# Performance work log

Measured on AMD Instinct MI355X. Metric: run time of the kernel, lower is better.

The kernel has to match this reference:

```python
import jax, jax.numpy as jnp
import numpy as np

B, S, D, H, DK = 32, 1024, 256, 8, 32
MASK_VALUE = -1e-30  # note: NOT -inf; masked scores become ~0 pre-softmax, faithful to source


def setup_inputs() -> dict:
    key = jax.random.key(0)
    ks = jax.random.split(key, 7)
    query = jax.random.normal(ks[0], (B, S, D), dtype=jnp.float32)
    key_t = jax.random.normal(ks[1], (B, S, D), dtype=jnp.float32)
    value = jax.random.normal(ks[2], (B, S, D), dtype=jnp.float32)
    # binary observation mask over key positions
    mask = (jax.random.uniform(ks[3], (B, S)) > 0.5).astype(jnp.float32)
    glorot = jax.nn.initializers.glorot_uniform(in_axis=1, out_axis=2)
    Wq = glorot(ks[4], (H, D, DK), jnp.float32)
    Wk = glorot(ks[5], (H, D, DK), jnp.float32)
    Wv = glorot(ks[6], (H, D, DK), jnp.float32)
    return {"query": query, "key": key_t, "value": value, "mask": mask,
            "Wq": Wq, "Wk": Wk, "Wv": Wv}


def reference(query, key, value, mask, Wq, Wk, Wv):
    # per-head projections, vectorized over heads: [B,S,D] x [H,D,DK] -> [B,H,S,DK]
    q = jnp.einsum('bsd,hdk->bhsk', query, Wq)
    k = jnp.einsum('bsd,hdk->bhsk', key, Wk)
    v = jnp.einsum('bsd,hdk->bhsk', value, Wv)
    # raw scores (no 1/sqrt(dk) scaling in source): [B,H,Sq,Sk]
    A = jnp.einsum('bhqk,bhsk->bhqs', q, k)
    m = mask[:, None, None, :]  # [B,1,1,Sk]
    A = m * A + (1.0 - m) * MASK_VALUE  # multiplicative mask, NOT additive
    A = jax.nn.softmax(A, axis=-1)
    out = jnp.einsum('bhqs,bhsk->bhqk', A, v)  # [B,H,Sq,DK]
    # concat heads along last dim, matching torch.cat order
    return out.transpose(0, 2, 1, 3).reshape(B, S, H * DK)
```

## Files before the change

### kernel.cpp

```cpp
#include <hip/hip_runtime.h>
#include <math.h>

#define B_  32
#define S_  1024
#define D_  256
#define H_  8
#define DK_ 32
#define MASKV (-1e-30f)
#define LOG2E 1.44269504f

typedef __attribute__((ext_vector_type(4))) short bf4_t;
typedef __attribute__((ext_vector_type(8))) short bf8_t;
typedef __attribute__((ext_vector_type(4))) float f4_t;

__device__ __forceinline__ unsigned fbits(float x) {
    union { float f; unsigned u; } v; v.f = x; return v.u;
}
__device__ __forceinline__ float bitsf(unsigned u) {
    union { unsigned u; float f; } v; v.u = u; return v.f;
}

#if __has_builtin(__builtin_amdgcn_exp2f)
#define EXP2F(x) __builtin_amdgcn_exp2f(x)
#else
#define EXP2F(x) __expf((x) * 0.69314718f)
#endif

__device__ __forceinline__ void gld16(const void* g, void* l) {
    __builtin_amdgcn_global_load_lds(
        (const __attribute__((address_space(1))) void*)g,
        (__attribute__((address_space(3))) void*)l, 16, 0, 0);
}

#define PSEL 0x07060302u

__global__ __launch_bounds__(256) void prep_w(
    const float* __restrict__ Wq, const float* __restrict__ Wk,
    const float* __restrict__ Wv, short* __restrict__ WtH, short* __restrict__ WtL)
{
    const int a = blockIdx.x >> 3;
    const int h = blockIdx.x & 7;
    const float* W = (a == 0 ? Wq : (a == 1 ? Wk : Wv)) + (size_t)h * 256 * 32;
    const int t = threadIdx.x;
    const int k    = t & 31;
    const int dgrp = t >> 5;
    short* th = WtH + ((size_t)a * 256 + h * 32 + k) * 256;
    short* tl = WtL + ((size_t)a * 256 + h * 32 + k) * 256;
#pragma unroll
    for (int jj = blockIdx.y * 2; jj < blockIdx.y * 2 + 2; ++jj) {
        const int d0 = jj * 32 + dgrp * 4;
        float x[4];
#pragma unroll
        for (int r = 0; r < 4; ++r) x[r] = W[(size_t)(d0 + r) * 32 + k];
        unsigned hu[4], lu[4];
#pragma unroll
        for (int r = 0; r < 4; ++r) {
            unsigned hb = (fbits(x[r]) + 0x8000u) & 0xFFFF0000u;
            hu[r] = hb;
            lu[r] = fbits(x[r] - bitsf(hb)) + 0x8000u;
        }
        uint2 hp = make_uint2(__builtin_amdgcn_perm(hu[1], hu[0], PSEL),
                              __builtin_amdgcn_perm(hu[3], hu[2], PSEL));
        uint2 lp = make_uint2(__builtin_amdgcn_perm(lu[1], lu[0], PSEL),
                              __builtin_amdgcn_perm(lu[3], lu[2], PSEL));
        *(uint2*)&th[d0] = hp;
        *(uint2*)&tl[d0] = lp;
    }
}

__global__ __launch_bounds__(256) void proj_kernel(
    const float* __restrict__ Xq, const float* __restrict__ Xk,
    const float* __restrict__ Xv,
    const short* __restrict__ WtH, const short* __restrict__ WtL,
    short* __restrict__ qpH, short* __restrict__ qpL,
    short* __restrict__ kpH, short* __restrict__ kpL,
    short* __restrict__ vpT)
{
    __shared__ __align__(16) short XsH[64 * 32];
    __shared__ __align__(16) short XsL[64 * 32];
    __shared__ __align__(16) short WsH[256 * 32];
    __shared__ __align__(16) short WsL[256 * 32];

    const int a  = blockIdx.y;
    const float* X = (a == 0 ? Xq : (a == 1 ? Xk : Xv));
    const short* WH = WtH + (size_t)a * 256 * 256;
    const short* WL = WtL + (size_t)a * 256 * 256;
    const int m0 = blockIdx.x * 64;

    const int tid  = threadIdx.x;
    const int lane = tid & 63;
    const int wv   = tid >> 6;
    const int l15  = lane & 15;
    const int quad = lane >> 4;

    f4_t acc[4][4];
#pragma unroll
    for (int i = 0; i < 4; ++i)
#pragma unroll
        for (int j = 0; j < 4; ++j) acc[i][j] = (f4_t){0.f, 0.f, 0.f, 0.f};

    for (int kc = 0; kc < 8; ++kc) {
        __syncthreads();
        {
            const float* xp = X + (size_t)(m0 + (tid >> 2)) * 256 + kc * 32 + (tid & 3) * 8;
            float4 x0 = *(const float4*)xp;
            float4 x1 = *(const float4*)(xp + 4);
            float xv[8] = {x0.x, x0.y, x0.z, x0.w, x1.x, x1.y, x1.z, x1.w};
            bf8_t hi, lo;
#pragma unroll
            for (int j = 0; j < 8; ++j) {
                unsigned hu = (fbits(xv[j]) + 0x8000u) & 0xFFFF0000u;
                hi[j] = (short)(hu >> 16);
                lo[j] = (short)((fbits(xv[j] - bitsf(hu)) + 0x8000u) >> 16);
            }
            *(bf8_t*)&XsH[(tid >> 2) * 32 + (tid & 3) * 8] = hi;
            *(bf8_t*)&XsL[(tid >> 2) * 32 + (tid & 3) * 8] = lo;
        }
#pragma unroll
        for (int i = 0; i < 4; ++i) {
            size_t go = (size_t)((i * 4 + wv) * 16 + (lane >> 2)) * 256 + kc * 32 + (lane & 3) * 8;
            gld16(WH + go, (char*)WsH + (i * 4 + wv) * 1024);
            gld16(WL + go, (char*)WsL + (i * 4 + wv) * 1024);
        }
        __syncthreads();

        bf8_t wH[4], wL[4];
#pragma unroll
        for (int ns = 0; ns < 4; ++ns) {
            int n = wv * 64 + ns * 16 + l15;
            wH[ns] = *(const bf8_t*)&WsH[n * 32 + quad * 8];
            wL[ns] = *(const bf8_t*)&WsL[n * 32 + quad * 8];
        }
#pragma unroll
        for (int t = 0; t < 4; ++t) {
            bf8_t xH = *(const bf8_t*)&XsH[(t * 16 + l15) * 32 + quad * 8];
            bf8_t xL = *(const bf8_t*)&XsL[(t * 16 + l15) * 32 + quad * 8];
#pragma unroll
            for (int ns = 0; ns < 4; ++ns) {
                f4_t c = acc[t][ns];
                if (a < 2) {
                    c = __builtin_amdgcn_mfma_f32_16x16x32_bf16(wH[ns], xH, c, 0, 0, 0);
                    c = __builtin_amdgcn_mfma_f32_16x16x32_bf16(wL[ns], xH, c, 0, 0, 0);
                    c = __builtin_amdgcn_mfma_f32_16x16x32_bf16(wH[ns], xL, c, 0, 0, 0);
                } else {
                    c = __builtin_amdgcn_mfma_f32_16x16x32_bf16(xH, wH[ns], c, 0, 0, 0);
                    c = __builtin_amdgcn_mfma_f32_16x16x32_bf16(xH, wL[ns], c, 0, 0, 0);
                    c = __builtin_amdgcn_mfma_f32_16x16x32_bf16(xL, wH[ns], c, 0, 0, 0);
                }
                acc[t][ns] = c;
            }
        }
    }

    const int b  = m0 >> 10;
    const int sB = m0 & 1023;
    if (a < 2) {
        short* dH = (a == 0) ? qpH : kpH;
        short* dL = (a == 0) ? qpL : kpL;
        const float scale = (a == 0) ? LOG2E : 1.0f;
#pragma unroll
        for (int t = 0; t < 4; ++t) {
            int s = sB + t * 16 + l15;
#pragma unroll
            for (int ns = 0; ns < 4; ++ns) {
                int nw = wv * 64 + ns * 16 + quad * 4;
                int h = nw >> 5, k0 = nw & 31;
                unsigned hu[4], lu[4];
#pragma unroll
                for (int r = 0; r < 4; ++r) {
                    float x = acc[t][ns][r] * scale;
                    unsigned h32 = fbits(x) + 0x8000u;
                    hu[r] = h32;
                    float hf = bitsf(h32 & 0xFFFF0000u);
                    lu[r] = fbits(x - hf) + 0x8000u;
                }
                uint2 hp = make_uint2(__builtin_amdgcn_perm(hu[1], hu[0], PSEL),
                                      __builtin_amdgcn_perm(hu[3], hu[2], PSEL));
                uint2 lp = make_uint2(__builtin_amdgcn_perm(lu[1], lu[0], PSEL),
                                      __builtin_amdgcn_perm(lu[3], lu[2], PSEL));
                size_t off = ((size_t)(b * 8 + h) * 1024 + s) * 32 + k0;
                *(uint2*)&dH[off] = hp;
                *(uint2*)&dL[off] = lp;
            }
        }
    } else {
#pragma unroll
        for (int t = 0; t < 4; ++t) {
            int sr = sB + t * 16 + quad * 4;
#pragma unroll
            for (int ns = 0; ns < 4; ++ns) {
                int n = wv * 64 + ns * 16 + l15;
                int h = n >> 5, k = n & 31;
                unsigned eu[4];
#pragma unroll
                for (int r = 0; r < 4; ++r) eu[r] = fbits(acc[t][ns][r]) + 0x8000u;
                uint2 pk = make_uint2(__builtin_amdgcn_perm(eu[1], eu[0], PSEL),
                                      __builtin_amdgcn_perm(eu[3], eu[2], PSEL));
                *(uint2*)&vpT[((size_t)(b * 8 + h) * 32 + k) * 1024 + sr] = pk;
            }
        }
    }
}

__global__ __launch_bounds__(256) void attn_kernel(
    const short* __restrict__ qpH, const short* __restrict__ qpL,
    const short* __restrict__ kpH, const short* __restrict__ kpL,
    const short* __restrict__ vpT, const float* __restrict__ mask,
    float* __restrict__ out)
{
    __shared__ __align__(16) short KsH[64 * 32];
    __shared__ __align__(16) short KsL[64 * 32];
    __shared__ __align__(16) short VsT[32 * 72];
    __shared__ __align__(16) float mskM[64];
    __shared__ __align__(16) float mskC[64];

    const int tid  = threadIdx.x;
    const int lane = tid & 63;
    const int wv   = tid >> 6;
    const int l15  = lane & 15;
    const int quad = lane >> 4;

    const int qt = blockIdx.x;
    const int h  = blockIdx.y;
    const int b  = blockIdx.z;
    const int bh = b * 8 + h;
    const int woff = qt * 128 + wv * 32;

    bf8_t qh[2], ql[2];
#pragma unroll
    for (int qs = 0; qs < 2; ++qs) {
        size_t row = (size_t)bh * 1024 + woff + qs * 16 + l15;
        qh[qs] = *(const bf8_t*)&qpH[row * 32 + quad * 8];
        ql[qs] = *(const bf8_t*)&qpL[row * 32 + quad * 8];
    }

    f4_t accO[2][2];
    f4_t accS[2];
#pragma unroll
    for (int i = 0; i < 2; ++i) {
        accS[i] = (f4_t){0.f, 0.f, 0.f, 0.f};
#pragma unroll
        for (int j = 0; j < 2; ++j) accO[i][j] = (f4_t){0.f, 0.f, 0.f, 0.f};
    }
    const bf4_t ones4 = {(short)0x3F80, (short)0x3F80, (short)0x3F80, (short)0x3F80};

    const float* mb = mask + (size_t)b * 1024;

    for (int kt = 0; kt < 16; ++kt) {
        __syncthreads();
        {
            size_t toff = ((size_t)bh * 1024 + kt * 64) * 32;
            gld16(kpH + toff + wv * 512 + lane * 8, (char*)KsH + wv * 1024);
            gld16(kpL + toff + wv * 512 + lane * 8, (char*)KsL + wv * 1024);
        }
        {
            int dv = tid >> 3, seg = tid & 7;
            const uint4 vvv = *(const uint4*)&vpT[((size_t)bh * 32 + dv) * 1024 + kt * 64 + seg * 8];
            *(uint4*)&VsT[dv * 72 + seg * 8] = vvv;
        }
        if (tid < 64) {
            float m = mb[kt * 64 + tid];
            mskM[tid] = m;
            mskC[tid] = (1.f - m) * (MASKV * LOG2E);
        }
        __syncthreads();

        f4_t sc[2][4];
#pragma unroll
        for (int ks = 0; ks < 4; ++ks) {
            bf8_t kh = *(const bf8_t*)&KsH[(ks * 16 + l15) * 32 + quad * 8];
            bf8_t kl = *(const bf8_t*)&KsL[(ks * 16 + l15) * 32 + quad * 8];
#pragma unroll
            for (int qs = 0; qs < 2; ++qs) {
                f4_t c = __builtin_amdgcn_mfma_f32_16x16x32_bf16(kh, qh[qs],
                             (f4_t){0.f, 0.f, 0.f, 0.f}, 0, 0, 0);
                c = __builtin_amdgcn_mfma_f32_16x16x32_bf16(kl, qh[qs], c, 0, 0, 0);
                c = __builtin_amdgcn_mfma_f32_16x16x32_bf16(kh, ql[qs], c, 0, 0, 0);
                sc[qs][ks] = c;
            }
        }

        bf4_t pf[2][4];
#pragma unroll
        for (int ks = 0; ks < 4; ++ks) {
            float4 m4 = *(const float4*)&mskM[ks * 16 + quad * 4];
            float4 c4 = *(const float4*)&mskC[ks * 16 + quad * 4];
            float mr[4] = {m4.x, m4.y, m4.z, m4.w};
            float cr[4] = {c4.x, c4.y, c4.z, c4.w};
#pragma unroll
            for (int qs = 0; qs < 2; ++qs) {
                unsigned eu[4];
#pragma unroll
                for (int r = 0; r < 4; ++r) {
                    float sm = fmaf(sc[qs][ks][r], mr[r], cr[r]);
                    eu[r] = fbits(EXP2F(sm)) + 0x8000u;
                }
                union { uint2 u; bf4_t v; } cv;
                cv.u = make_uint2(__builtin_amdgcn_perm(eu[1], eu[0], PSEL),
                                  __builtin_amdgcn_perm(eu[3], eu[2], PSEL));
                pf[qs][ks] = cv.v;
            }
        }

#pragma unroll
        for (int ks = 0; ks < 4; ++ks) {
            bf4_t vf0 = *(const bf4_t*)&VsT[l15 * 72 + ks * 16 + quad * 4];
            bf4_t vf1 = *(const bf4_t*)&VsT[(16 + l15) * 72 + ks * 16 + quad * 4];
#pragma unroll
            for (int qs = 0; qs < 2; ++qs) {
                accO[qs][0] = __builtin_amdgcn_mfma_f32_16x16x16bf16_1k(vf0, pf[qs][ks], accO[qs][0], 0, 0, 0);
                accO[qs][1] = __builtin_amdgcn_mfma_f32_16x16x16bf16_1k(vf1, pf[qs][ks], accO[qs][1], 0, 0, 0);
                accS[qs]    = __builtin_amdgcn_mfma_f32_16x16x16bf16_1k(ones4, pf[qs][ks], accS[qs], 0, 0, 0);
            }
        }
    }

#pragma unroll
    for (int qs = 0; qs < 2; ++qs) {
        float inv = 1.0f / accS[qs][0];
        int s = woff + qs * 16 + l15;
        float* op = out + ((size_t)b * 1024 + s) * 256 + h * 32;
#pragma unroll
        for (int dvs = 0; dvs < 2; ++dvs) {
            float4 o4 = make_float4(accO[qs][dvs][0] * inv, accO[qs][dvs][1] * inv,
                                    accO[qs][dvs][2] * inv, accO[qs][dvs][3] * inv);
            *(float4*)&op[dvs * 16 + quad * 4] = o4;
        }
    }
}

extern "C" void kernel_launch(void* const* d_in, const int* in_sizes, int n_in,
                              void* d_out, int out_size, void* d_ws, size_t ws_size,
                              hipStream_t stream)
{
    const float* query = (const float*)d_in[0];
    const float* key   = (const float*)d_in[1];
    const float* value = (const float*)d_in[2];
    const float* mask  = (const float*)d_in[3];
    const float* Wq    = (const float*)d_in[4];
    const float* Wk    = (const float*)d_in[5];
    const float* Wv    = (const float*)d_in[6];
    float* out = (float*)d_out;

    const size_t per = (size_t)B_ * H_ * S_ * DK_;
    short* qpH = (short*)d_ws;
    short* qpL = qpH + per;
    short* kpH = qpL + per;
    short* kpL = kpH + per;
    short* vpT = kpL + per;
    short* WtH = vpT + per;
    short* WtL = WtH + 3 * 256 * 256;

    prep_w<<<dim3(24, 4), 256, 0, stream>>>(Wq, Wk, Wv, WtH, WtL);
    proj_kernel<<<dim3(512, 3), 256, 0, stream>>>(query, key, value, WtH, WtL,
                                                  qpH, qpL, kpH, kpL, vpT);
    attn_kernel<<<dim3(8, H_, B_), 256, 0, stream>>>(qpH, qpL, kpH, kpL, vpT, mask, out);
}
```

Measured before the change: 284.2 us.

## Fold key mask into K projection and double-buffer K/V tiles in attention

The key mask is now multiplied into the K projection output inside proj_kernel. The attention kernel therefore drops its per-tile mask loads and the mask FMA. Masked scores become exactly 0 instead of roughly -1e-30, which gives the same exp2 result. The attention loop now double-buffers the K/V shared tiles, prefetching the next tile while computing on the current one, which doubles shared memory per block. The block index is also remapped to change scheduling order, and the weight async loads are issued before the X conversion in the projection.

```diff
diff --git a/kernel.cpp b/kernel.cpp
--- a/kernel.cpp
+++ b/kernel.cpp
@@ -70,7 +70,7 @@
 
 __global__ __launch_bounds__(256) void proj_kernel(
     const float* __restrict__ Xq, const float* __restrict__ Xk,
-    const float* __restrict__ Xv,
+    const float* __restrict__ Xv, const float* __restrict__ mask,
     const short* __restrict__ WtH, const short* __restrict__ WtL,
     short* __restrict__ qpH, short* __restrict__ qpL,
     short* __restrict__ kpH, short* __restrict__ kpL,
@@ -101,6 +101,12 @@
 
     for (int kc = 0; kc < 8; ++kc) {
         __syncthreads();
+#pragma unroll
+        for (int i = 0; i < 4; ++i) {
+            size_t go = (size_t)((i * 4 + wv) * 16 + (lane >> 2)) * 256 + kc * 32 + (lane & 3) * 8;
+            gld16(WH + go, (char*)WsH + (i * 4 + wv) * 1024);
+            gld16(WL + go, (char*)WsL + (i * 4 + wv) * 1024);
+        }
         {
             const float* xp = X + (size_t)(m0 + (tid >> 2)) * 256 + kc * 32 + (tid & 3) * 8;
             float4 x0 = *(const float4*)xp;
@@ -115,12 +121,6 @@
             }
             *(bf8_t*)&XsH[(tid >> 2) * 32 + (tid & 3) * 8] = hi;
             *(bf8_t*)&XsL[(tid >> 2) * 32 + (tid & 3) * 8] = lo;
-        }
-#pragma unroll
-        for (int i = 0; i < 4; ++i) {
-            size_t go = (size_t)((i * 4 + wv) * 16 + (lane >> 2)) * 256 + kc * 32 + (lane & 3) * 8;
-            gld16(WH + go, (char*)WsH + (i * 4 + wv) * 1024);
-            gld16(WL + go, (char*)WsL + (i * 4 + wv) * 1024);
         }
         __syncthreads();
 
@@ -157,10 +157,11 @@
     if (a < 2) {
         short* dH = (a == 0) ? qpH : kpH;
         short* dL = (a == 0) ? qpL : kpL;
-        const float scale = (a == 0) ? LOG2E : 1.0f;
+        const float* mbp = mask + (size_t)b * 1024;
 #pragma unroll
         for (int t = 0; t < 4; ++t) {
             int s = sB + t * 16 + l15;
+            const float scale = (a == 0) ? LOG2E : mbp[s];
 #pragma unroll
             for (int ns = 0; ns < 4; ++ns) {
                 int nw = wv * 64 + ns * 16 + quad * 4;
@@ -205,14 +206,11 @@
 __global__ __launch_bounds__(256) void attn_kernel(
     const short* __restrict__ qpH, const short* __restrict__ qpL,
     const short* __restrict__ kpH, const short* __restrict__ kpL,
-    const short* __restrict__ vpT, const float* __restrict__ mask,
-    float* __restrict__ out)
+    const short* __restrict__ vpT, float* __restrict__ out)
 {
-    __shared__ __align__(16) short KsH[64 * 32];
-    __shared__ __align__(16) short KsL[64 * 32];
-    __shared__ __align__(16) short VsT[32 * 72];
-    __shared__ __align__(16) float mskM[64];
-    __shared__ __align__(16) float mskC[64];
+    __shared__ __align__(16) short KsH[2][64 * 32];
+    __shared__ __align__(16) short KsL[2][64 * 32];
+    __shared__ __align__(16) short VsT[2][32 * 72];
 
     const int tid  = threadIdx.x;
     const int lane = tid & 63;
@@ -220,10 +218,12 @@
     const int l15  = lane & 15;
     const int quad = lane >> 4;
 
-    const int qt = blockIdx.x;
-    const int h  = blockIdx.y;
-    const int b  = blockIdx.z;
-    const int bh = b * 8 + h;
+    const int L  = (blockIdx.z * gridDim.y + blockIdx.y) * gridDim.x + blockIdx.x;
+    const int li = L >> 3;
+    const int bh = (L & 7) * 32 + (li >> 3);
+    const int qt = li & 7;
+    const int b  = bh >> 3;
+    const int h  = bh & 7;
     const int woff = qt * 128 + wv * 32;
 
     bf8_t qh[2], ql[2];
@@ -244,32 +244,34 @@
     }
     const bf4_t ones4 = {(short)0x3F80, (short)0x3F80, (short)0x3F80, (short)0x3F80};
 
-    const float* mb = mask + (size_t)b * 1024;
-
+    const int dv = tid >> 3, seg = tid & 7;
+
+    {
+        size_t toff = ((size_t)bh * 1024) * 32;
+        gld16(kpH + toff + wv * 512 + lane * 8, (char*)KsH[0] + wv * 1024);
+        gld16(kpL + toff + wv * 512 + lane * 8, (char*)KsL[0] + wv * 1024);
+        uint4 v0 = *(const uint4*)&vpT[((size_t)bh * 32 + dv) * 1024 + seg * 8];
+        *(uint4*)&VsT[0][dv * 72 + seg * 8] = v0;
+    }
+    __syncthreads();
+
+    int cur = 0;
     for (int kt = 0; kt < 16; ++kt) {
-        __syncthreads();
-        {
-            size_t toff = ((size_t)bh * 1024 + kt * 64) * 32;
-            gld16(kpH + toff + wv * 512 + lane * 8, (char*)KsH + wv * 1024);
-            gld16(kpL + toff + wv * 512 + lane * 8, (char*)KsL + wv * 1024);
-        }
-        {
-            int dv = tid >> 3, seg = tid & 7;
-            const uint4 vvv = *(const uint4*)&vpT[((size_t)bh * 32 + dv) * 1024 + kt * 64 + seg * 8];
-            *(uint4*)&VsT[dv * 72 + seg * 8] = vvv;
-        }
-        if (tid < 64) {
-            float m = mb[kt * 64 + tid];
-            mskM[tid] = m;
-            mskC[tid] = (1.f - m) * (MASKV * LOG2E);
-        }
-        __syncthreads();
+        const int nxt = cur ^ 1;
+
+        uint4 vreg;
+        if (kt < 15) {
+            size_t toff = ((size_t)bh * 1024 + (kt + 1) * 64) * 32;
+            gld16(kpH + toff + wv * 512 + lane * 8, (char*)KsH[nxt] + wv * 1024);
+            gld16(kpL + toff + wv * 512 + lane * 8, (char*)KsL[nxt] + wv * 1024);
+            vreg = *(const uint4*)&vpT[((size_t)bh * 32 + dv) * 1024 + (kt + 1) * 64 + seg * 8];
+        }
 
         f4_t sc[2][4];
 #pragma unroll
         for (int ks = 0; ks < 4; ++ks) {
-            bf8_t kh = *(const bf8_t*)&KsH[(ks * 16 + l15) * 32 + quad * 8];
-            bf8_t kl = *(const bf8_t*)&KsL[(ks * 16 + l15) * 32 + quad * 8];
+            bf8_t kh = *(const bf8_t*)&KsH[cur][(ks * 16 + l15) * 32 + quad * 8];
+            bf8_t kl = *(const bf8_t*)&KsL[cur][(ks * 16 + l15) * 32 + quad * 8];
 #pragma unroll
             for (int qs = 0; qs < 2; ++qs) {
                 f4_t c = __builtin_amdgcn_mfma_f32_16x16x32_bf16(kh, qh[qs],
@@ -283,18 +285,12 @@
         bf4_t pf[2][4];
 #pragma unroll
         for (int ks = 0; ks < 4; ++ks) {
-            float4 m4 = *(const float4*)&mskM[ks * 16 + quad * 4];
-            float4 c4 = *(const float4*)&mskC[ks * 16 + quad * 4];
-            float mr[4] = {m4.x, m4.y, m4.z, m4.w};
-            float cr[4] = {c4.x, c4.y, c4.z, c4.w};
 #pragma unroll
             for (int qs = 0; qs < 2; ++qs) {
                 unsigned eu[4];
 #pragma unroll
-                for (int r = 0; r < 4; ++r) {
-                    float sm = fmaf(sc[qs][ks][r], mr[r], cr[r]);
-                    eu[r] = fbits(EXP2F(sm)) + 0x8000u;
-                }
+                for (int r = 0; r < 4; ++r)
+                    eu[r] = fbits(EXP2F(sc[qs][ks][r])) + 0x8000u;
                 union { uint2 u; bf4_t v; } cv;
                 cv.u = make_uint2(__builtin_amdgcn_perm(eu[1], eu[0], PSEL),
                                   __builtin_amdgcn_perm(eu[3], eu[2], PSEL));
@@ -304,8 +300,8 @@
 
 #pragma unroll
         for (int ks = 0; ks < 4; ++ks) {
-            bf4_t vf0 = *(const bf4_t*)&VsT[l15 * 72 + ks * 16 + quad * 4];
-            bf4_t vf1 = *(const bf4_t*)&VsT[(16 + l15) * 72 + ks * 16 + quad * 4];
+            bf4_t vf0 = *(const bf4_t*)&VsT[cur][l15 * 72 + ks * 16 + quad * 4];
+            bf4_t vf1 = *(const bf4_t*)&VsT[cur][(16 + l15) * 72 + ks * 16 + quad * 4];
 #pragma unroll
             for (int qs = 0; qs < 2; ++qs) {
                 accO[qs][0] = __builtin_amdgcn_mfma_f32_16x16x16bf16_1k(vf0, pf[qs][ks], accO[qs][0], 0, 0, 0);
@@ -313,6 +309,10 @@
                 accS[qs]    = __builtin_amdgcn_mfma_f32_16x16x16bf16_1k(ones4, pf[qs][ks], accS[qs], 0, 0, 0);
             }
         }
+
+        if (kt < 15) *(uint4*)&VsT[nxt][dv * 72 + seg * 8] = vreg;
+        __syncthreads();
+        cur = nxt;
     }
 
 #pragma unroll
@@ -352,7 +352,7 @@
     short* WtL = WtH + 3 * 256 * 256;
 
     prep_w<<<dim3(24, 4), 256, 0, stream>>>(Wq, Wk, Wv, WtH, WtL);
-    proj_kernel<<<dim3(512, 3), 256, 0, stream>>>(query, key, value, WtH, WtL,
+    proj_kernel<<<dim3(512, 3), 256, 0, stream>>>(query, key, value, mask, WtH, WtL,
                                                   qpH, qpL, kpH, kpL, vpT);
-    attn_kernel<<<dim3(8, H_, B_), 256, 0, stream>>>(qpH, qpL, kpH, kpL, vpT, mask, out);
-}
+    attn_kernel<<<dim3(8, H_, B_), 256, 0, stream>>>(qpH, qpL, kpH, kpL, vpT, out);
+}
```

Measured after the change: 279.0 us. About the same (-1.8%).
